# Performance work log

Hardware: AMD Instinct MI355X
Metric: run time of the kernel (lower is better)

The kernel has to match this reference:

```python
import jax, jax.numpy as jnp
import numpy as np

B, S, HID = 2, 2048, 2048
NH, NKV, HD = 16, 16, 128
SCALE = 1.0 / np.sqrt(HD)


def _rotate_half(x):
    x1, x2 = jnp.split(x, 2, axis=-1)
    return jnp.concatenate([-x2, x1], axis=-1)


def setup_inputs() -> dict:
    key = jax.random.key(0)
    k1, k2, k3 = jax.random.split(key, 3)
    hidden_states = jax.random.normal(k1, (B, S, HID), dtype=jnp.float32)
    # standard RoPE cos/sin tables, shape [S, HD]
    inv_freq = 1.0 / (10000.0 ** (np.arange(0, HD, 2, dtype=np.float32) / HD))
    freqs = np.outer(np.arange(S, dtype=np.float32), inv_freq)  # [S, HD/2]
    emb = np.concatenate([freqs, freqs], axis=-1)               # [S, HD]
    cos = jnp.asarray(np.cos(emb), dtype=jnp.float32)
    sin = jnp.asarray(np.sin(emb), dtype=jnp.float32)
    # torch Linear weights are [out, in]; forward computes x @ W.T
    w_qkv = jax.random.normal(k2, ((NH + 2 * NKV) * HD, HID), dtype=jnp.float32) * 0.02
    w_o = jax.random.normal(k3, (HID, NH * HD), dtype=jnp.float32) * 0.02
    return {"hidden_states": hidden_states, "cos": cos, "sin": sin,
            "w_qkv": w_qkv, "w_o": w_o}


def reference(hidden_states, cos, sin, w_qkv, w_o):
    b, s, _ = hidden_states.shape
    qkv = hidden_states @ w_qkv.T                         # [B,S,(NH+2*NKV)*HD]
    qkv = qkv.reshape(b, s, NH + 2 * NKV, HD)
    q = qkv[:, :, :NH]                                    # [B,S,NH,HD]
    k = qkv[:, :, NH:NH + NKV]                            # [B,S,NKV,HD]
    v = qkv[:, :, NH + NKV:]                              # [B,S,NKV,HD]
    # RoPE: broadcast cos/sin [S,HD] -> [1,S,1,HD]
    c = cos[None, :, None, :]
    sn = sin[None, :, None, :]
    q = q * c + _rotate_half(q) * sn
    k = k * c + _rotate_half(k) * sn
    scores = jnp.einsum("bihd,bjhd->bhij", q, k) * SCALE  # [B,H,S,S]
    attn = jax.nn.softmax(scores, axis=-1)
    out = jnp.einsum("bhij,bjhd->bihd", attn, v)          # [B,S,H,HD]
    out = out.reshape(b, s, NH * HD)
    return out @ w_o.T                                    # [B,S,HID]
```

## Files before the change

kernel.cpp:

```cpp
#include <hip/hip_runtime.h>
#include <hip/hip_bf16.h>

typedef float f32x4 __attribute__((ext_vector_type(4)));
typedef __bf16 bf16x8 __attribute__((ext_vector_type(8)));
typedef __bf16 bf16x4 __attribute__((ext_vector_type(4)));

#define S_LEN 2048
#define NHEADS 16
#define HDIM 128
#define KLOG2E (0.08838834764831845f * 1.4426950408889634f)
#define MSHIFT 2.0f

__device__ __forceinline__ void gld_lds16(const __bf16* g, __bf16* l) {
  __builtin_amdgcn_global_load_lds(
      (__attribute__((address_space(1))) void*)(void*)g,
      (__attribute__((address_space(3))) void*)l,
      16, 0, 0);
}

template <int N>
__device__ __forceinline__ void waitv() {
  if constexpr (N == 8)      asm volatile("s_waitcnt vmcnt(8)" ::: "memory");
  else if constexpr (N == 6) asm volatile("s_waitcnt vmcnt(6)" ::: "memory");
  else if constexpr (N == 4) asm volatile("s_waitcnt vmcnt(4)" ::: "memory");
  else if constexpr (N == 3) asm volatile("s_waitcnt vmcnt(3)" ::: "memory");
  else                       asm volatile("s_waitcnt vmcnt(0)" ::: "memory");
}

__global__ __launch_bounds__(256)
void cvt_all(const float* __restrict__ i0, __bf16* __restrict__ o0,
             const float* __restrict__ i1, __bf16* __restrict__ o1,
             const float* __restrict__ i2, __bf16* __restrict__ o2) {
  int i = (blockIdx.x * 256 + threadIdx.x) * 4;
  if (i >= 25165824) return;
  const float* in;
  __bf16* out;
  if (i < 8388608)       { in = i0 + i;              out = o0 + i; }
  else if (i < 20971520) { in = i1 + (i - 8388608);  out = o1 + (i - 8388608); }
  else                   { in = i2 + (i - 20971520); out = o2 + (i - 20971520); }
  float4 v = *(const float4*)in;
  bf16x4 o;
  o[0] = (__bf16)v.x; o[1] = (__bf16)v.y; o[2] = (__bf16)v.z; o[3] = (__bf16)v.w;
  *(bf16x4*)out = o;
}

template <int MREP, bool RMAP>
__device__ __forceinline__ void gemm_core(const __bf16* __restrict__ A,
                                          const __bf16* __restrict__ B,
                                          __bf16* lds, int am0, int bn0,
                                          f32x4 (&acc)[MREP][4]) {
  constexpr int K = 2048;
  constexpr int AF = MREP * 2;
  constexpr int SLOT = (AF + 16) * 512;
  constexpr int NA = AF / 8;
  constexpr int NL = NA + 2;
  const int tid = threadIdx.x;
  const int w = tid >> 6, lane = tid & 63;
  const int l15 = lane & 15;
  const int wm = w >> 2, wn = w & 3;

  const __bf16* asrc = A + (size_t)(am0 + l15) * K + (lane >> 4) * 8;
  const __bf16* bsrc = B + (size_t)(bn0 + l15) * K + (lane >> 4) * 8;

  auto stage = [&](int t) {
    __bf16* s = lds + (t & 3) * SLOT;
#pragma unroll
    for (int i = 0; i < NA; ++i) {
      const int f = w * NA + i;
      gld_lds16(asrc + (size_t)f * (16 * K) + t * 32, s + f * 512 + lane * 8);
    }
#pragma unroll
    for (int i = 0; i < 2; ++i) {
      const int g = w * 2 + i;
      gld_lds16(bsrc + (size_t)g * (16 * K) + t * 32, s + (AF + g) * 512 + lane * 8);
    }
  };

  stage(0); stage(1); stage(2);
  waitv<2 * NL>();
  __builtin_amdgcn_s_barrier();

  for (int t = 0; t < 64; ++t) {
    if (t < 61) stage(t + 3);
    const __bf16* s = lds + (t & 3) * SLOT + lane * 8;
    const __bf16* sB = s + AF * 512;
    bf16x8 bfr[4];
#pragma unroll
    for (int j = 0; j < 4; ++j) {
      const int g = RMAP ? ((wn >> 1) * 8 + (wn & 1) * 2 + (j & 1) + (j >> 1) * 4)
                         : (wn * 4 + j);
      bfr[j] = *(const bf16x8*)(sB + g * 512);
    }
#pragma unroll
    for (int half = 0; half < MREP / 4; ++half) {
      bf16x8 af[4];
#pragma unroll
      for (int i = 0; i < 4; ++i)
        af[i] = *(const bf16x8*)(s + (wm * MREP + half * 4 + i) * 512);
      __builtin_amdgcn_s_setprio(1);
#pragma unroll
      for (int i = 0; i < 4; ++i)
#pragma unroll
        for (int j = 0; j < 4; ++j)
          acc[half * 4 + i][j] = __builtin_amdgcn_mfma_f32_16x16x32_bf16(
              af[i], bfr[j], acc[half * 4 + i][j], 0, 0, 0);
      __builtin_amdgcn_s_setprio(0);
    }
    if (t < 63) {
      if (t < 61)       waitv<2 * NL>();
      else if (t == 61) waitv<NL>();
      else              waitv<0>();
      __builtin_amdgcn_s_barrier();
    }
  }
}


__global__ __launch_bounds__(512)
void gemm_bt_qkp(const __bf16* __restrict__ A, const __bf16* __restrict__ B,
                 __bf16* __restrict__ Qp, __bf16* __restrict__ Kp,
                 const float* __restrict__ cosp, const float* __restrict__ sinp) {
  __shared__ alignas(16) char smem[139264];
  const int am0 = blockIdx.y * 256;
  const int bn0 = blockIdx.x * 256;
  const int tid = threadIdx.x;
  const int w = tid >> 6, lane = tid & 63;
  const int l15 = lane & 15, quad = lane >> 4;
  const int wm = w >> 2, wn = w & 3;
  f32x4 acc[8][4] = {};
  gemm_core<8, true>(A, B, (__bf16*)smem, am0, bn0, acc);

  __syncthreads();
  float* csb = (float*)smem;
  float* snb = csb + 256 * 68;
  const int sbase = am0 & 2047;
  for (int q = tid; q < 4096; q += 512) {
    const int row = q >> 4, dq = (q & 15) * 4;
    *(float4*)(csb + row * 68 + dq) =
        *(const float4*)(cosp + (size_t)(sbase + row) * 128 + dq);
    *(float4*)(snb + row * 68 + dq) =
        *(const float4*)(sinp + (size_t)(sbase + row) * 128 + dq);
  }
  __syncthreads();

  const int head_sel = wn >> 1;
  const int hcol0 = bn0 + head_sel * 128;
  const int head = hcol0 >> 7;
  const int h = head & 15;
  __bf16* dst = (head < 16) ? Qp : Kp;
#pragma unroll
  for (int i = 0; i < 8; ++i) {
    const int row_b = am0 + wm * 128 + i * 16 + quad * 4;
    const int bidx = row_b >> 11;
    const int s = row_b & 2047;
    const int sl = wm * 128 + i * 16 + quad * 4;
    const int s16 = s >> 4;
    const int l15p0 = s & 15;
#pragma unroll
    for (int j2 = 0; j2 < 2; ++j2) {
      const int dl = (wn & 1) * 32 + j2 * 16 + l15;
      const int dh = dl + 64;
      const int kkl = dl >> 5, qpl = (dl >> 3) & 3, el = dl & 7;
      const int kkh = dh >> 5, qph = (dh >> 3) & 3, eh = dh & 7;
      const size_t base_lo =
          (((size_t)((bidx * 16 + h) * 128 + s16) * 4 + kkl) * 64 + qpl * 16 + l15p0) * 8 + el;
      const size_t base_hi =
          (((size_t)((bidx * 16 + h) * 128 + s16) * 4 + kkh) * 64 + qph * 16 + l15p0) * 8 + eh;
#pragma unroll
      for (int r = 0; r < 4; ++r) {
        const float c = csb[(sl + r) * 68 + dl];
        const float sn = snb[(sl + r) * 68 + dl];
        const float a = acc[i][j2][r], bb = acc[i][j2 + 2][r];
        dst[base_lo + (size_t)r * 8] = (__bf16)(a * c - bb * sn);
        dst[base_hi + (size_t)r * 8] = (__bf16)(bb * c + a * sn);
      }
    }
  }
}

__global__ __launch_bounds__(512)
void gemm_bt_vp(const __bf16* __restrict__ A, const __bf16* __restrict__ B,
                __bf16* __restrict__ Vp) {
  __shared__ alignas(16) __bf16 lds[4 * 24 * 512];
  const int am0 = blockIdx.y * 128;
  const int bn0 = blockIdx.x * 256;
  const int tid = threadIdx.x;
  const int w = tid >> 6, lane = tid & 63;
  const int l15 = lane & 15, quad = lane >> 4;
  const int wm = w >> 2, wn = w & 3;
  f32x4 acc[4][4] = {};
  gemm_core<4, false>(A, B, lds, am0, bn0, acc);
#pragma unroll
  for (int i = 0; i < 4; ++i) {
    const int row_b = am0 + wm * 64 + i * 16 + quad * 4;
    const int b = row_b >> 11;
    const int key0 = row_b & 2047;
    const int quadp = (key0 >> 3) & 3;
    const int kkv = key0 >> 5;
    const int e0 = key0 & 7;
#pragma unroll
    for (int j = 0; j < 4; ++j) {
      const int col = bn0 + wn * 64 + j * 16 + l15;
      const int h = col >> 7, dd = col & 127;
      const int tt = dd >> 4, l15p = dd & 15;
      bf16x4 o;
#pragma unroll
      for (int r = 0; r < 4; ++r) o[r] = (__bf16)acc[i][j][r];
      size_t addr = (((size_t)((b * 16 + h) * 8 + tt) * 64 + kkv) * 64
                     + quadp * 16 + l15p) * 8 + e0;
      *(bf16x4*)(Vp + addr) = o;
    }
  }
}

__global__ __launch_bounds__(512)
void gemm_bt_f(const __bf16* __restrict__ A, const __bf16* __restrict__ B,
               float* __restrict__ C) {
  __shared__ alignas(16) __bf16 lds[4 * 24 * 512];
  const int am0 = blockIdx.y * 128;
  const int bn0 = blockIdx.x * 256;
  const int tid = threadIdx.x;
  const int w = tid >> 6, lane = tid & 63;
  const int l15 = lane & 15, quad = lane >> 4;
  const int wm = w >> 2, wn = w & 3;
  f32x4 acc[4][4] = {};
  gemm_core<4, false>(A, B, lds, am0, bn0, acc);
#pragma unroll
  for (int i = 0; i < 4; ++i) {
    const int row_b = am0 + wm * 64 + i * 16 + quad * 4;
#pragma unroll
    for (int j = 0; j < 4; ++j) {
      const int col = bn0 + wn * 64 + j * 16 + l15;
#pragma unroll
      for (int r = 0; r < 4; ++r)
        C[(size_t)(row_b + r) * 2048 + col] = acc[i][j][r];
    }
  }
}

__global__ __launch_bounds__(256, 2)
void attn_kernel(const __bf16* __restrict__ Qp, const __bf16* __restrict__ Kp,
                 const __bf16* __restrict__ Vp, __bf16* __restrict__ O) {
  const int lid = blockIdx.x;
  const int qt = (lid >> 3) & 15;
  const int bh = (lid & 7) * 4 + (lid >> 7);
  const int b = bh >> 4, h = bh & 15;
  const int tid = threadIdx.x;
  const int w = tid >> 6;
  const int lane = tid & 63;
  const int l15 = lane & 15, quad = lane >> 4;

  __shared__ alignas(16) __bf16 Kls[2][16 * 512];
  __shared__ alignas(16) __bf16 Vls[2][16 * 512];
  __shared__ alignas(16) __bf16 Ps[4][16 * 64];

  const __bf16* qbase = Qp + (size_t)bh * 262144 + lane * 8;
  const __bf16* kbase = Kp + (size_t)bh * 262144 + lane * 8;
  const __bf16* vbase = Vp + (size_t)bh * 262144 + lane * 8;

  bf16x8 qf[2][4];
#pragma unroll
  for (int qb = 0; qb < 2; ++qb)
#pragma unroll
    for (int kk = 0; kk < 4; ++kk)
      qf[qb][kk] =
          *(const bf16x8*)(qbase + (size_t)((qt * 8 + qb * 4 + w) * 4 + kk) * 512);

  bf16x8 onesf;
#pragma unroll
  for (int e = 0; e < 8; ++e) onesf[e] = (__bf16)1.0f;

  f32x4 o_acc[2][8] = {};
  f32x4 o_sum[2] = {};

  const int swz = (l15 & 7) << 3;
  __bf16* psw = &Ps[w][l15 * 64];

  auto stage = [&](int tile) {
    __bf16* ks = &Kls[tile & 1][0];
    __bf16* vs = &Vls[tile & 1][0];
#pragma unroll
    for (int ii = 0; ii < 4; ++ii) {
      const int c = w * 4 + ii;
      gld_lds16(kbase + ((size_t)tile * 16 + c) * 512, ks + c * 512 + lane * 8);
    }
#pragma unroll
    for (int ii = 0; ii < 4; ++ii) {
      const int c = w * 4 + ii;
      gld_lds16(vbase + (size_t)((c >> 1) * 64 + tile * 2 + (c & 1)) * 512,
                vs + c * 512 + lane * 8);
    }
  };

  stage(0);
  waitv<4>();
  __builtin_amdgcn_s_barrier();

  for (int t = 0; t < 32; ++t) {
    const __bf16* ks = &Kls[t & 1][0] + lane * 8;
    const __bf16* vs = &Vls[t & 1][0] + lane * 8;

    bf16x8 kf[16];
#pragma unroll
    for (int f = 0; f < 16; ++f)
      kf[f] = *(const bf16x8*)(ks + f * 512);

    f32x4 sc[2][4] = {};
    __builtin_amdgcn_s_setprio(1);
#pragma unroll
    for (int kk = 0; kk < 4; ++kk)
#pragma unroll
      for (int tt = 0; tt < 4; ++tt)
        sc[0][tt] = __builtin_amdgcn_mfma_f32_16x16x32_bf16(
            kf[tt * 4 + kk], qf[0][kk], sc[0][tt], 0, 0, 0);
#pragma unroll
    for (int kk = 0; kk < 4; ++kk)
#pragma unroll
      for (int tt = 0; tt < 4; ++tt)
        sc[1][tt] = __builtin_amdgcn_mfma_f32_16x16x32_bf16(
            kf[tt * 4 + kk], qf[1][kk], sc[1][tt], 0, 0, 0);
    __builtin_amdgcn_s_setprio(0);

    bf16x8 pa0[2], pa1[2];
#pragma unroll
    for (int tt = 0; tt < 4; ++tt) {
      bf16x4 o;
#pragma unroll
      for (int r = 0; r < 4; ++r)
        o[r] = (__bf16)__builtin_amdgcn_exp2f(
            __builtin_fmaf(sc[0][tt][r], KLOG2E, -MSHIFT));
      *(bf16x4*)(psw + ((tt * 16 + quad * 4) ^ swz)) = o;
    }
    pa0[0] = *(const bf16x8*)(psw + ((quad * 8) ^ swz));
    pa0[1] = *(const bf16x8*)(psw + ((32 + quad * 8) ^ swz));

    waitv<0>();
    __builtin_amdgcn_s_barrier();
    if (t < 31) stage(t + 1);

    bf16x8 vf[16];
#pragma unroll
    for (int f = 0; f < 16; ++f)
      vf[f] = *(const bf16x8*)(vs + f * 512);

    __builtin_amdgcn_s_setprio(1);
#pragma unroll
    for (int kk = 0; kk < 2; ++kk) {
      o_sum[0] = __builtin_amdgcn_mfma_f32_16x16x32_bf16(pa0[kk], onesf, o_sum[0], 0, 0, 0);
#pragma unroll
      for (int tt = 0; tt < 8; ++tt)
        o_acc[0][tt] = __builtin_amdgcn_mfma_f32_16x16x32_bf16(
            pa0[kk], vf[tt * 2 + kk], o_acc[0][tt], 0, 0, 0);
    }
    __builtin_amdgcn_s_setprio(0);

#pragma unroll
    for (int tt = 0; tt < 4; ++tt) {
      bf16x4 o;
#pragma unroll
      for (int r = 0; r < 4; ++r)
        o[r] = (__bf16)__builtin_amdgcn_exp2f(
            __builtin_fmaf(sc[1][tt][r], KLOG2E, -MSHIFT));
      *(bf16x4*)(psw + ((tt * 16 + quad * 4) ^ swz)) = o;
    }
    pa1[0] = *(const bf16x8*)(psw + ((quad * 8) ^ swz));
    pa1[1] = *(const bf16x8*)(psw + ((32 + quad * 8) ^ swz));

    __builtin_amdgcn_s_setprio(1);
#pragma unroll
    for (int kk = 0; kk < 2; ++kk) {
      o_sum[1] = __builtin_amdgcn_mfma_f32_16x16x32_bf16(pa1[kk], onesf, o_sum[1], 0, 0, 0);
#pragma unroll
      for (int tt = 0; tt < 8; ++tt)
        o_acc[1][tt] = __builtin_amdgcn_mfma_f32_16x16x32_bf16(
            pa1[kk], vf[tt * 2 + kk], o_acc[1][tt], 0, 0, 0);
    }
    __builtin_amdgcn_s_setprio(0);

    if (t < 31) {
      waitv<4>();
      __builtin_amdgcn_s_barrier();
    }
  }

#pragma unroll
  for (int qb = 0; qb < 2; ++qb) {
    float inv[4];
#pragma unroll
    for (int r = 0; r < 4; ++r) inv[r] = 1.0f / o_sum[qb][r];
    const int row0 = qt * 128 + (qb * 4 + w) * 16 + quad * 4;
#pragma unroll
    for (int tt = 0; tt < 8; ++tt)
#pragma unroll
      for (int r = 0; r < 4; ++r)
        O[(size_t)(b * S_LEN + row0 + r) * 2048 + h * HDIM + tt * 16 + l15] =
            (__bf16)(o_acc[qb][tt][r] * inv[r]);
  }
}

extern "C" void kernel_launch(void* const* d_in, const int* in_sizes, int n_in,
                              void* d_out, int out_size, void* d_ws, size_t ws_size,
                              hipStream_t stream) {
  const float* hs   = (const float*)d_in[0];
  const float* cosp = (const float*)d_in[1];
  const float* sinp = (const float*)d_in[2];
  const float* wqkv = (const float*)d_in[3];
  const float* wo   = (const float*)d_in[4];
  float* out = (float*)d_out;

  char* ws = (char*)d_ws;
  __bf16* Xb   = (__bf16*)(ws);
  __bf16* Obuf = (__bf16*)(ws);
  __bf16* Wqb  = (__bf16*)(ws + 16777216);
  __bf16* Wob  = (__bf16*)(ws + 41943040);
  __bf16* Qp   = (__bf16*)(ws + 50331648);
  __bf16* Kp   = (__bf16*)(ws + 67108864);
  __bf16* Vp   = (__bf16*)(ws + 83886080);
  if (ws_size < 100663296) return;

  cvt_all<<<24576, 256, 0, stream>>>(hs, Xb, wqkv, Wqb, wo, Wob);

  gemm_bt_qkp<<<dim3(16, 16), 512, 0, stream>>>(Xb, Wqb, Qp, Kp, cosp, sinp);
  gemm_bt_vp<<<dim3(8, 32), 512, 0, stream>>>(Xb, Wqb + 8388608, Vp);
  attn_kernel<<<512, 256, 0, stream>>>(Qp, Kp, Vp, Obuf);
  gemm_bt_f<<<dim3(8, 32), 512, 0, stream>>>(Obuf, Wob, out);
}
```

Measured before the change: 389.6 us.

## Interleave global-to-LDS prefetch with LDS fragment reads and MFMA phases in GEMM core

Splits the prefetch stage into separate A and B parts and issues them after each phase's LDS fragment reads rather than at the top of the iteration. For MREP==8 it splits each k-step into two barrier-fenced phases, issuing the A prefetch in the first and the B prefetch in the second. This spreads memory issue across the MFMA work so loads and LDS reads overlap more evenly with compute. In exchange it adds extra s_barrier and lgkmcnt(0) waits per iteration, which can stall waves.

```diff
diff --git a/kernel.cpp b/kernel.cpp
--- a/kernel.cpp
+++ b/kernel.cpp
@@ -25,6 +25,11 @@
   else if constexpr (N == 4) asm volatile("s_waitcnt vmcnt(4)" ::: "memory");
   else if constexpr (N == 3) asm volatile("s_waitcnt vmcnt(3)" ::: "memory");
   else                       asm volatile("s_waitcnt vmcnt(0)" ::: "memory");
+}
+
+__device__ __forceinline__ void lgkm0_fence() {
+  asm volatile("s_waitcnt lgkmcnt(0)" ::: "memory");
+  __builtin_amdgcn_sched_barrier(0);
 }
 
 __global__ __launch_bounds__(256)
@@ -62,13 +67,16 @@
   const __bf16* asrc = A + (size_t)(am0 + l15) * K + (lane >> 4) * 8;
   const __bf16* bsrc = B + (size_t)(bn0 + l15) * K + (lane >> 4) * 8;
 
-  auto stage = [&](int t) {
+  auto stageA = [&](int t) {
     __bf16* s = lds + (t & 3) * SLOT;
 #pragma unroll
     for (int i = 0; i < NA; ++i) {
       const int f = w * NA + i;
       gld_lds16(asrc + (size_t)f * (16 * K) + t * 32, s + f * 512 + lane * 8);
     }
+  };
+  auto stageB = [&](int t) {
+    __bf16* s = lds + (t & 3) * SLOT;
 #pragma unroll
     for (int i = 0; i < 2; ++i) {
       const int g = w * 2 + i;
@@ -76,14 +84,14 @@
     }
   };
 
-  stage(0); stage(1); stage(2);
+  stageA(0); stageB(0); stageA(1); stageB(1); stageA(2); stageB(2);
   waitv<2 * NL>();
   __builtin_amdgcn_s_barrier();
 
   for (int t = 0; t < 64; ++t) {
-    if (t < 61) stage(t + 3);
     const __bf16* s = lds + (t & 3) * SLOT + lane * 8;
     const __bf16* sB = s + AF * 512;
+
     bf16x8 bfr[4];
 #pragma unroll
     for (int j = 0; j < 4; ++j) {
@@ -91,21 +99,44 @@
                          : (wn * 4 + j);
       bfr[j] = *(const bf16x8*)(sB + g * 512);
     }
-#pragma unroll
-    for (int half = 0; half < MREP / 4; ++half) {
-      bf16x8 af[4];
+    bf16x8 af[4];
+#pragma unroll
+    for (int i = 0; i < 4; ++i)
+      af[i] = *(const bf16x8*)(s + (wm * MREP + i) * 512);
+    if (t < 61) {
+      stageA(t + 3);
+      if constexpr (MREP == 4) stageB(t + 3);
+    }
+    __builtin_amdgcn_s_barrier();
+    lgkm0_fence();
+    __builtin_amdgcn_s_setprio(1);
+#pragma unroll
+    for (int i = 0; i < 4; ++i)
+#pragma unroll
+      for (int j = 0; j < 4; ++j)
+        acc[i][j] = __builtin_amdgcn_mfma_f32_16x16x32_bf16(
+            af[i], bfr[j], acc[i][j], 0, 0, 0);
+    __builtin_amdgcn_s_setprio(0);
+
+    if constexpr (MREP == 8) {
+      __builtin_amdgcn_s_barrier();
+      bf16x8 af2[4];
 #pragma unroll
       for (int i = 0; i < 4; ++i)
-        af[i] = *(const bf16x8*)(s + (wm * MREP + half * 4 + i) * 512);
+        af2[i] = *(const bf16x8*)(s + (wm * MREP + 4 + i) * 512);
+      if (t < 61) stageB(t + 3);
+      __builtin_amdgcn_s_barrier();
+      lgkm0_fence();
       __builtin_amdgcn_s_setprio(1);
 #pragma unroll
       for (int i = 0; i < 4; ++i)
 #pragma unroll
         for (int j = 0; j < 4; ++j)
-          acc[half * 4 + i][j] = __builtin_amdgcn_mfma_f32_16x16x32_bf16(
-              af[i], bfr[j], acc[half * 4 + i][j], 0, 0, 0);
+          acc[4 + i][j] = __builtin_amdgcn_mfma_f32_16x16x32_bf16(
+              af2[i], bfr[j], acc[4 + i][j], 0, 0, 0);
       __builtin_amdgcn_s_setprio(0);
     }
+
     if (t < 63) {
       if (t < 61)       waitv<2 * NL>();
       else if (t == 61) waitv<NL>();
```

Result: no change. 389.3 us (-0.1%).

## Switch GEMM core to double-buffered K=64 stages with explicit LDS wait fence

Applied to the files above, without the earlier changes.

The shared GEMM mainloop moves from a 4-slot ring of K=32 stages with prefetch depth 3 to a 2-slot ring of K=64 stages with prefetch depth 1, so there are half as many iterations and barriers. Each iteration now handles two K-halves, loading all A fragments at once and issuing an explicit lgkmcnt(0) wait plus sched_barrier before the MFMA block. Per-iteration LDS usage doubles but the slot count halves, so total LDS per block is unchanged for the V and output GEMMs. The shallower prefetch and the full vmcnt(0) wait every iteration may expose more global-load latency. The QK GEMM's LDS buffer (139264 bytes) is not resized, which appears to match the new slot layout for MREP=8.

```diff
diff --git a/kernel.cpp b/kernel.cpp
--- a/kernel.cpp
+++ b/kernel.cpp
@@ -25,6 +25,11 @@
   else if constexpr (N == 4) asm volatile("s_waitcnt vmcnt(4)" ::: "memory");
   else if constexpr (N == 3) asm volatile("s_waitcnt vmcnt(3)" ::: "memory");
   else                       asm volatile("s_waitcnt vmcnt(0)" ::: "memory");
+}
+
+__device__ __forceinline__ void lgkm0_fence() {
+  asm volatile("s_waitcnt lgkmcnt(0)" ::: "memory");
+  __builtin_amdgcn_sched_barrier(0);
 }
 
 __global__ __launch_bounds__(256)
@@ -50,10 +55,9 @@
                                           __bf16* lds, int am0, int bn0,
                                           f32x4 (&acc)[MREP][4]) {
   constexpr int K = 2048;
-  constexpr int AF = MREP * 2;
-  constexpr int SLOT = (AF + 16) * 512;
-  constexpr int NA = AF / 8;
-  constexpr int NL = NA + 2;
+  constexpr int AFRAG = MREP * 4;
+  constexpr int SLOT = (AFRAG + 32) * 512;
+  constexpr int NA = MREP / 2;
   const int tid = threadIdx.x;
   const int w = tid >> 6, lane = tid & 63;
   const int l15 = lane & 15;
@@ -63,53 +67,54 @@
   const __bf16* bsrc = B + (size_t)(bn0 + l15) * K + (lane >> 4) * 8;
 
   auto stage = [&](int t) {
-    __bf16* s = lds + (t & 3) * SLOT;
+    __bf16* s = lds + (t & 1) * SLOT;
 #pragma unroll
     for (int i = 0; i < NA; ++i) {
-      const int f = w * NA + i;
-      gld_lds16(asrc + (size_t)f * (16 * K) + t * 32, s + f * 512 + lane * 8);
-    }
-#pragma unroll
-    for (int i = 0; i < 2; ++i) {
-      const int g = w * 2 + i;
-      gld_lds16(bsrc + (size_t)g * (16 * K) + t * 32, s + (AF + g) * 512 + lane * 8);
+      const int fi = w * NA + i;
+      gld_lds16(asrc + (size_t)(fi >> 1) * (16 * K) + t * 64 + (fi & 1) * 32,
+                s + fi * 512 + lane * 8);
+    }
+#pragma unroll
+    for (int i = 0; i < 4; ++i) {
+      const int gi = w * 4 + i;
+      gld_lds16(bsrc + (size_t)(gi >> 1) * (16 * K) + t * 64 + (gi & 1) * 32,
+                s + (AFRAG + gi) * 512 + lane * 8);
     }
   };
 
-  stage(0); stage(1); stage(2);
-  waitv<2 * NL>();
+  stage(0);
+  waitv<0>();
   __builtin_amdgcn_s_barrier();
 
-  for (int t = 0; t < 64; ++t) {
-    if (t < 61) stage(t + 3);
-    const __bf16* s = lds + (t & 3) * SLOT + lane * 8;
-    const __bf16* sB = s + AF * 512;
-    bf16x8 bfr[4];
-#pragma unroll
-    for (int j = 0; j < 4; ++j) {
-      const int g = RMAP ? ((wn >> 1) * 8 + (wn & 1) * 2 + (j & 1) + (j >> 1) * 4)
-                         : (wn * 4 + j);
-      bfr[j] = *(const bf16x8*)(sB + g * 512);
-    }
-#pragma unroll
-    for (int half = 0; half < MREP / 4; ++half) {
-      bf16x8 af[4];
-#pragma unroll
-      for (int i = 0; i < 4; ++i)
-        af[i] = *(const bf16x8*)(s + (wm * MREP + half * 4 + i) * 512);
+  for (int t = 0; t < 32; ++t) {
+    if (t < 31) stage(t + 1);
+    const __bf16* s = lds + (t & 1) * SLOT + lane * 8;
+    const __bf16* sB = s + AFRAG * 512;
+#pragma unroll
+    for (int kh = 0; kh < 2; ++kh) {
+      bf16x8 bfr[4];
+#pragma unroll
+      for (int j = 0; j < 4; ++j) {
+        const int g = RMAP ? ((wn >> 1) * 8 + (wn & 1) * 2 + (j & 1) + (j >> 1) * 4)
+                           : (wn * 4 + j);
+        bfr[j] = *(const bf16x8*)(sB + (g * 2 + kh) * 512);
+      }
+      bf16x8 af[MREP];
+#pragma unroll
+      for (int i = 0; i < MREP; ++i)
+        af[i] = *(const bf16x8*)(s + ((wm * MREP + i) * 2 + kh) * 512);
+      lgkm0_fence();
       __builtin_amdgcn_s_setprio(1);
 #pragma unroll
-      for (int i = 0; i < 4; ++i)
+      for (int i = 0; i < MREP; ++i)
 #pragma unroll
         for (int j = 0; j < 4; ++j)
-          acc[half * 4 + i][j] = __builtin_amdgcn_mfma_f32_16x16x32_bf16(
-              af[i], bfr[j], acc[half * 4 + i][j], 0, 0, 0);
+          acc[i][j] = __builtin_amdgcn_mfma_f32_16x16x32_bf16(
+              af[i], bfr[j], acc[i][j], 0, 0, 0);
       __builtin_amdgcn_s_setprio(0);
     }
-    if (t < 63) {
-      if (t < 61)       waitv<2 * NL>();
-      else if (t == 61) waitv<NL>();
-      else              waitv<0>();
+    if (t < 31) {
+      waitv<0>();
       __builtin_amdgcn_s_barrier();
     }
   }
@@ -181,7 +186,7 @@
 __global__ __launch_bounds__(512)
 void gemm_bt_vp(const __bf16* __restrict__ A, const __bf16* __restrict__ B,
                 __bf16* __restrict__ Vp) {
-  __shared__ alignas(16) __bf16 lds[4 * 24 * 512];
+  __shared__ alignas(16) __bf16 lds[2 * 48 * 512];
   const int am0 = blockIdx.y * 128;
   const int bn0 = blockIdx.x * 256;
   const int tid = threadIdx.x;
@@ -216,7 +221,7 @@
 __global__ __launch_bounds__(512)
 void gemm_bt_f(const __bf16* __restrict__ A, const __bf16* __restrict__ B,
                float* __restrict__ C) {
-  __shared__ alignas(16) __bf16 lds[4 * 24 * 512];
+  __shared__ alignas(16) __bf16 lds[2 * 48 * 512];
   const int am0 = blockIdx.y * 128;
   const int bn0 = blockIdx.x * 256;
   const int tid = threadIdx.x;
```

Result: slower. 416.5 us (+6.9%).
